# Performance work log

Hardware: AMD Instinct MI355X
Metric: run time of the kernel (lower is better)

## Reference

```python
import math
import jax, jax.numpy as jnp
import numpy as np

B, T, S = 4, 4096, 1024
HID, CTX, EMB, H = 1024, 768, 1024, 16
D = EMB // H  # head_dim = 64


def setup_inputs() -> dict:
    key = jax.random.key(0)
    ks = jax.random.split(key, 7)
    sc = lambda n: 1.0 / math.sqrt(n)
    return {
        "tokens": jax.random.normal(ks[0], (B, T, HID), jnp.float32),
        "context": jax.random.normal(ks[1], (B, S, CTX), jnp.float32),
        "Wq": jax.random.normal(ks[2], (HID, EMB), jnp.float32) * sc(HID),
        "Wk": jax.random.normal(ks[3], (CTX, EMB), jnp.float32) * sc(CTX),
        "Wv": jax.random.normal(ks[4], (CTX, EMB), jnp.float32) * sc(CTX),
        "Wo": jax.random.normal(ks[5], (EMB, HID), jnp.float32) * sc(EMB),
        "bo": jnp.zeros((HID,), jnp.float32),
    }


def reference(tokens, context, Wq, Wk, Wv, Wo, bo):
    # projections (bias-free, as in torch Linear(bias=False))
    Q = tokens @ Wq              # [B,T,EMB]
    K = context @ Wk             # [B,S,EMB]
    V = context @ Wv             # [B,S,EMB]
    # split heads: B T (H D) -> B H T D
    Q = Q.reshape(B, T, H, D).transpose(0, 2, 1, 3)
    K = K.reshape(B, S, H, D).transpose(0, 2, 1, 3)
    V = V.reshape(B, S, H, D).transpose(0, 2, 1, 3)
    scores = jnp.einsum('bhtd,bhsd->bhts', Q, K) / math.sqrt(D)
    attn = jax.nn.softmax(scores, axis=-1)
    ctx = jnp.einsum('bhts,bhsd->bhtd', attn, V)
    ctx = ctx.transpose(0, 2, 1, 3).reshape(B, T, EMB)
    return ctx @ Wo + bo
```

## Files before the change

kernel.cpp:

```cpp
#include <hip/hip_runtime.h>
#include <hip/hip_bf16.h>

#define B_ 4
#define T_ 4096
#define S_ 1024
#define HID_ 1024
#define CTX_ 768
#define EMB_ 1024
#define H_ 16
#define D_ 64

#define QSCALE 0.18033688011112042f

typedef __attribute__((ext_vector_type(8))) short short8;
typedef __attribute__((ext_vector_type(4))) float f32x4;
typedef __attribute__((ext_vector_type(4))) unsigned short us4;
typedef unsigned short ushort_t;

__device__ inline ushort_t f2b(float f) {
  union { float f; unsigned u; } x; x.f = f;
  return (ushort_t)((x.u + 0x7fffu + ((x.u >> 16) & 1u)) >> 16);
}
__device__ inline unsigned cvtpk2(float a, float b) {
  __hip_bfloat162 h = __float22bfloat162_rn(float2{a, b});
  union { __hip_bfloat162 h; unsigned u; } c; c.h = h; return c.u;
}
__device__ inline ushort_t f2b_fast(float f) {
  __hip_bfloat16 h = __float2bfloat16(f);
  union { __hip_bfloat16 h; ushort_t u; } c; c.h = h; return c.u;
}

using gu32p = const __attribute__((address_space(1))) unsigned int*;
using lu32p = __attribute__((address_space(3))) unsigned int*;
__device__ inline void gload16(const ushort_t* g, ushort_t* l) {
  __builtin_amdgcn_global_load_lds((gu32p)(const void*)g, (lu32p)(void*)l, 16, 0, 0);
}

__device__ inline void conv_body(const float* __restrict__ in, ushort_t* __restrict__ out,
                                 int blk, int tid) {
  const size_t i = ((size_t)blk * 256 + tid) * 8;
  const float4 a = *(const float4*)(in + i);
  const float4 b = *(const float4*)(in + i + 4);
  uint4 u;
  u.x = cvtpk2(a.x, a.y); u.y = cvtpk2(a.z, a.w);
  u.z = cvtpk2(b.x, b.y); u.w = cvtpk2(b.z, b.w);
  *(uint4*)(out + i) = u;
}

__device__ inline void convT_body(const float* __restrict__ W, ushort_t* __restrict__ Wt,
                                  int K, int tile, int tid, float (*Ls)[33]) {
  const int n0 = (tile & 31) * 32, k0 = (tile >> 5) * 32;
  const int r = tid >> 3, c4 = (tid & 7) * 4;
  const float4 v = *(const float4*)&W[(size_t)(k0 + r) * 1024 + n0 + c4];
  Ls[r][c4] = v.x; Ls[r][c4 + 1] = v.y; Ls[r][c4 + 2] = v.z; Ls[r][c4 + 3] = v.w;
  __syncthreads();
  us4 o;
  o.x = f2b_fast(Ls[c4][r]);     o.y = f2b_fast(Ls[c4 + 1][r]);
  o.z = f2b_fast(Ls[c4 + 2][r]); o.w = f2b_fast(Ls[c4 + 3][r]);
  *(us4*)&Wt[(size_t)(n0 + r) * K + k0 + c4] = o;
}

__global__ __launch_bounds__(256) void prepA(
    const float* __restrict__ context,
    const float* __restrict__ Wq, const float* __restrict__ Wk,
    const float* __restrict__ Wv, const float* __restrict__ Wo,
    ushort_t* __restrict__ CtxB, ushort_t* __restrict__ WqT,
    ushort_t* __restrict__ WkvT, ushort_t* __restrict__ WoT)
{
  __shared__ float Ls[32][33];
  const int tid = threadIdx.x;
  int blk = (int)blockIdx.x;
  if (blk < 1536) { conv_body(context, CtxB, blk, tid); return; }
  blk -= 1536;
  if (blk < 1024) { convT_body(Wq, WqT, 1024, blk, tid, Ls); return; }
  blk -= 1024;
  if (blk < 768)  { convT_body(Wk, WkvT, 768, blk, tid, Ls); return; }
  blk -= 768;
  if (blk < 768)  { convT_body(Wv, WkvT + (size_t)1024 * 768, 768, blk, tid, Ls); return; }
  blk -= 768;
  convT_body(Wo, WoT, 1024, blk, tid, Ls);
}

__global__ __launch_bounds__(512) void gemm256kv(
    const ushort_t* __restrict__ A, const ushort_t* __restrict__ Bt,
    ushort_t* __restrict__ Kb, ushort_t* __restrict__ Vtb)
{
  constexpr int Kd = CTX_, NT = CTX_ / 32;
  extern __shared__ ushort_t L[];
  const int tid = threadIdx.x;
  const int lane = tid & 63, wid = tid >> 6;
  const int lr = lane & 15, lg = lane >> 4;
  const int wm = wid >> 2, wn = wid & 3;

  const int lin = (int)blockIdx.x;
  const int swz = (lin & 7) * 32 + (lin >> 3);
  const int bm = swz >> 3, bn = swz & 7;

  const int sr = tid >> 2;
  const int csrc = (tid & 3) ^ ((sr >> 1) & 3);
  const ushort_t* gA = A + (size_t)(bm * 128 + sr) * Kd + csrc * 8;
  const ushort_t* gB = Bt + (size_t)(bn * 256 + sr) * Kd + csrc * 8;
  const size_t halfB = (size_t)128 * Kd;

  f32x4 acc[4][4] = {};

#define KVSTAGE(c, slot) do { const int k0_ = (c) << 5;            \
    ushort_t* s_ = L + (slot) * 12288;                             \
    gload16(gA + k0_, s_ + tid * 8);                               \
    gload16(gB + k0_, s_ + 4096 + tid * 8);                        \
    gload16(gB + k0_ + halfB, s_ + 8192 + tid * 8);                \
  } while (0)

  KVSTAGE(0, 0); KVSTAGE(1, 1);
  int cur = 0, sls = 2;
  for (int t = 0; t < NT; ++t) {
    if (t < NT - 1) asm volatile("s_waitcnt vmcnt(3)" ::: "memory");
    else            asm volatile("s_waitcnt vmcnt(0)" ::: "memory");
    __builtin_amdgcn_s_barrier();
    __builtin_amdgcn_sched_barrier(0);
    if (t + 2 < NT) KVSTAGE(t + 2, sls);
    const ushort_t* As_ = L + cur * 12288;
    const ushort_t* Bs_ = As_ + 4096;
    short8 af[4], bf[4];
#pragma unroll
    for (int m = 0; m < 4; ++m) {
      const int row = wm * 64 + m * 16 + lr;
      af[m] = *(const short8*)&As_[row * 32 + (lg ^ ((row >> 1) & 3)) * 8];
    }
#pragma unroll
    for (int n = 0; n < 4; ++n) {
      const int row = wn * 64 + n * 16 + lr;
      bf[n] = *(const short8*)&Bs_[row * 32 + (lg ^ ((row >> 1) & 3)) * 8];
    }
    __builtin_amdgcn_s_setprio(1);
#pragma unroll
    for (int m = 0; m < 4; ++m)
#pragma unroll
      for (int n = 0; n < 4; ++n)
        acc[m][n] = __builtin_amdgcn_mfma_f32_16x16x32_bf16(af[m], bf[n], acc[m][n], 0, 0, 0);
    __builtin_amdgcn_s_setprio(0);
    cur = (cur == 2) ? 0 : cur + 1;
    sls = (sls == 2) ? 0 : sls + 1;
  }
#undef KVSTAGE

  const int row0 = bm * 128 + wm * 64 + lg * 4;
  const int col0 = bn * 256 + wn * 64 + lr;

  if (col0 < 1024) {
#pragma unroll
    for (int m = 0; m < 4; ++m)
#pragma unroll
      for (int n = 0; n < 4; ++n) {
        const int col = col0 + n * 16;
#pragma unroll
        for (int i = 0; i < 4; ++i)
          Kb[(size_t)(row0 + m * 16 + i) * EMB_ + col] = f2b_fast(acc[m][n][i]);
      }
  } else {
#pragma unroll
    for (int m = 0; m < 4; ++m) {
      const int rbase = row0 + m * 16;
      const int bb = rbase >> 10;
      const int s0 = rbase & (S_ - 1);
#pragma unroll
      for (int n = 0; n < 4; ++n) {
        const int vc = col0 + n * 16 - 1024;
        const int hh = vc >> 6, dd = vc & 63;
        us4 o;
        o.x = f2b_fast(acc[m][n][0]); o.y = f2b_fast(acc[m][n][1]);
        o.z = f2b_fast(acc[m][n][2]); o.w = f2b_fast(acc[m][n][3]);
        *(us4*)&Vtb[(((size_t)bb * H_ + hh) * D_ + dd) * S_ + s0] = o;
      }
    }
  }
}

__global__ __launch_bounds__(512) void gemm256p(
    const ushort_t* __restrict__ A, const ushort_t* __restrict__ Bt,
    float* __restrict__ Cp, const float* __restrict__ bias,
    int M, int Kd, int N)
{
  extern __shared__ ushort_t L[];
  const int tid = threadIdx.x;
  const int lane = tid & 63, wid = tid >> 6;
  const int lr = lane & 15, lg = lane >> 4;
  const int wm = wid >> 2, wn = wid & 3;

  const int cpx = (int)gridDim.x >> 3;
  const int lin = (int)blockIdx.x;
  const int swz = (lin & 7) * cpx + (lin >> 3);
  const int nbn = N >> 8;
  const int bm = swz / nbn, bn = swz % nbn;

  const int sr = tid >> 2;
  const int csrc = (tid & 3) ^ ((sr >> 1) & 3);
  const ushort_t* gA = A + (size_t)(bm * 256 + sr) * Kd + csrc * 8;
  const ushort_t* gB = Bt + (size_t)(bn * 256 + sr) * Kd + csrc * 8;
  const size_t half = (size_t)128 * Kd;

  f32x4 acc[8][4] = {};
  const int NT = Kd >> 5;

#define STAGEQ(c, q) do {                                            \
    const int k0_ = (c) << 5;                                        \
    ushort_t* s_ = L + ((c) % 3) * 16384 + (q) * 4096 + tid * 8;     \
    if ((q) == 0)      gload16(gA + k0_, s_);                        \
    else if ((q) == 1) gload16(gA + k0_ + half, s_);                 \
    else if ((q) == 2) gload16(gB + k0_, s_);                        \
    else               gload16(gB + k0_ + half, s_);                 \
  } while (0)

#pragma unroll
  for (int q = 0; q < 4; ++q) STAGEQ(0, q);
#pragma unroll
  for (int q = 0; q < 4; ++q) STAGEQ(1, q);
  asm volatile("s_waitcnt vmcnt(4)" ::: "memory");
  __builtin_amdgcn_s_barrier();
  __builtin_amdgcn_sched_barrier(0);

  for (int t = 0; t < NT; ++t) {
    const ushort_t* As_ = L + (t % 3) * 16384;
    const ushort_t* Bs_ = As_ + 8192;
    const bool st = (t + 2 < NT);
    short8 bf[4];
#pragma unroll
    for (int q = 0; q < 4; ++q) {
      if (q == 0) {
#pragma unroll
        for (int n = 0; n < 4; ++n) {
          const int row = wn * 64 + n * 16 + lr;
          bf[n] = *(const short8*)&Bs_[row * 32 + (lg ^ ((row >> 1) & 3)) * 8];
        }
      }
      const int r0 = wm * 128 + (2 * q) * 16 + lr;
      const int r1 = r0 + 16;
      const short8 af0 = *(const short8*)&As_[r0 * 32 + (lg ^ ((r0 >> 1) & 3)) * 8];
      const short8 af1 = *(const short8*)&As_[r1 * 32 + (lg ^ ((r1 >> 1) & 3)) * 8];
      if (st) STAGEQ(t + 2, q);
      __builtin_amdgcn_s_barrier();
      asm volatile("s_waitcnt lgkmcnt(0)" ::: "memory");
      __builtin_amdgcn_sched_barrier(0);
      __builtin_amdgcn_s_setprio(1);
#pragma unroll
      for (int n = 0; n < 4; ++n)
        acc[2 * q][n] = __builtin_amdgcn_mfma_f32_16x16x32_bf16(af0, bf[n], acc[2 * q][n], 0, 0, 0);
#pragma unroll
      for (int n = 0; n < 4; ++n)
        acc[2 * q + 1][n] = __builtin_amdgcn_mfma_f32_16x16x32_bf16(af1, bf[n], acc[2 * q + 1][n], 0, 0, 0);
      __builtin_amdgcn_s_setprio(0);
      if (q == 3 && t < NT - 1) {
        if (st) asm volatile("s_waitcnt vmcnt(4)" ::: "memory");
        else    asm volatile("s_waitcnt vmcnt(0)" ::: "memory");
      }
      __builtin_amdgcn_s_barrier();
      __builtin_amdgcn_sched_barrier(0);
    }
  }
#undef STAGEQ

  const int row0 = bm * 256 + wm * 128 + lg * 4;
  const int col0 = bn * 256 + wn * 64 + lr;
#pragma unroll
  for (int n = 0; n < 4; ++n) {
    const int col = col0 + n * 16;
    const float bv = bias[col];
#pragma unroll
    for (int m = 0; m < 8; ++m)
#pragma unroll
      for (int i = 0; i < 4; ++i)
        Cp[(size_t)(row0 + m * 16 + i) * N + col] = acc[m][n][i] + bv;
  }
}

__global__ __launch_bounds__(512) void gemm256f(
    const float* __restrict__ Af, const ushort_t* __restrict__ Bt,
    ushort_t* __restrict__ Cp, int M, int N)
{
  constexpr int Kd = 1024, NT = 32;
  extern __shared__ ushort_t L[];
  const int tid = threadIdx.x;
  const int lane = tid & 63, wid = tid >> 6;
  const int lr = lane & 15, lg = lane >> 4;
  const int wm = wid >> 2, wn = wid & 3;

  const int cpx = (int)gridDim.x >> 3;
  const int lin = (int)blockIdx.x;
  const int swz = (lin & 7) * cpx + (lin >> 3);
  const int nbn = N >> 8;
  const int bm = swz / nbn, bn = swz % nbn;

  const int sr = tid >> 2;
  const int csrc = (tid & 3) ^ ((sr >> 1) & 3);
  const float* gA = Af + (size_t)(bm * 256 + sr) * Kd + csrc * 8;
  const ushort_t* gB = Bt + (size_t)(bn * 256 + sr) * Kd + csrc * 8;
  const size_t half = (size_t)128 * Kd;
  ushort_t* const dA = L + tid * 8;
  ushort_t* const dB = L + 8192 + tid * 8;

  f32x4 acc[8][4] = {};
  float4 ra0[4], ra1[4];

#define ALOADF(c, RS) do { const int k0_ = (c) << 5;      \
    RS[0] = *(const float4*)(gA + k0_);                   \
    RS[1] = *(const float4*)(gA + k0_ + 4);               \
    RS[2] = *(const float4*)(gA + k0_ + half);            \
    RS[3] = *(const float4*)(gA + k0_ + half + 4);        \
  } while (0)

#define AWRITE(c, RS) do { const int slot_ = ((c) & 3) * 16384;  \
    uint4 u0, u1;                                                \
    u0.x = cvtpk2(RS[0].x, RS[0].y); u0.y = cvtpk2(RS[0].z, RS[0].w); \
    u0.z = cvtpk2(RS[1].x, RS[1].y); u0.w = cvtpk2(RS[1].z, RS[1].w); \
    u1.x = cvtpk2(RS[2].x, RS[2].y); u1.y = cvtpk2(RS[2].z, RS[2].w); \
    u1.z = cvtpk2(RS[3].x, RS[3].y); u1.w = cvtpk2(RS[3].z, RS[3].w); \
    *(uint4*)(dA + slot_) = u0;                                  \
    *(uint4*)(dA + slot_ + 4096) = u1;                           \
  } while (0)

#define BSTAGE(c) do { const int slot_ = ((c) & 3) * 16384; const int k0_ = (c) << 5; \
    gload16(gB + k0_, dB + slot_);                      \
    gload16(gB + k0_ + half, dB + slot_ + 4096);        \
  } while (0)

#define COMPUTE(c) do {                                                  \
    const ushort_t* As_ = L + ((c) & 3) * 16384;                         \
    const ushort_t* Bs_ = As_ + 8192;                                    \
    short8 af[8], bf[4];                                                 \
    _Pragma("unroll")                                                    \
    for (int m = 0; m < 8; ++m) {                                        \
      const int row = wm * 128 + m * 16 + lr;                            \
      af[m] = *(const short8*)&As_[row * 32 + (lg ^ ((row >> 1) & 3)) * 8]; \
    }                                                                    \
    _Pragma("unroll")                                                    \
    for (int n = 0; n < 4; ++n) {                                        \
      const int row = wn * 64 + n * 16 + lr;                             \
      bf[n] = *(const short8*)&Bs_[row * 32 + (lg ^ ((row >> 1) & 3)) * 8]; \
    }                                                                    \
    __builtin_amdgcn_s_setprio(1);                                       \
    _Pragma("unroll")                                                    \
    for (int m = 0; m < 8; ++m)                                          \
      _Pragma("unroll")                                                  \
      for (int n = 0; n < 4; ++n)                                        \
        acc[m][n] = __builtin_amdgcn_mfma_f32_16x16x32_bf16(af[m], bf[n], acc[m][n], 0, 0, 0); \
    __builtin_amdgcn_s_setprio(0);                                       \
  } while (0)

#define ENDBAR do {                                        \
    asm volatile("s_waitcnt lgkmcnt(0)" ::: "memory");     \
    __builtin_amdgcn_s_barrier();                          \
    __builtin_amdgcn_sched_barrier(0);                     \
  } while (0)

  {
    float4 p0[4], p1[4], p2[4];
    ALOADF(0, p0); ALOADF(1, p1); ALOADF(2, p2);
    AWRITE(0, p0); AWRITE(1, p1); AWRITE(2, p2);
    BSTAGE(0); BSTAGE(1); BSTAGE(2);
    ALOADF(3, ra1);
    asm volatile("s_waitcnt vmcnt(4)" ::: "memory");
    ENDBAR;
  }

  for (int t = 0; t < NT; t += 2) {
    if (t + 3 < NT) { AWRITE(t + 3, ra1); BSTAGE(t + 3); }
    if (t + 4 < NT) ALOADF(t + 4, ra0);
    COMPUTE(t);
    ENDBAR;
    if (t + 4 < NT) { AWRITE(t + 4, ra0); BSTAGE(t + 4); }
    if (t + 5 < NT) ALOADF(t + 5, ra1);
    COMPUTE(t + 1);
    ENDBAR;
  }
#undef ALOADF
#undef AWRITE
#undef BSTAGE
#undef COMPUTE
#undef ENDBAR

  const int row0 = bm * 256 + wm * 128 + lg * 4;
  const int col0 = bn * 256 + wn * 64 + lr;
#pragma unroll
  for (int m = 0; m < 8; ++m)
#pragma unroll
    for (int n = 0; n < 4; ++n) {
      const int col = col0 + n * 16;
#pragma unroll
      for (int i = 0; i < 4; ++i)
        Cp[(size_t)(row0 + m * 16 + i) * N + col] = f2b(acc[m][n][i] * QSCALE);
    }
}

__global__ __launch_bounds__(512) void attn_v8(
    const ushort_t* __restrict__ Q, const ushort_t* __restrict__ K,
    const ushort_t* __restrict__ Vt, ushort_t* __restrict__ C)
{
  extern __shared__ ushort_t SM[];
  const int tid = threadIdx.x;
  const int lane = tid & 63, w = tid >> 6;
  const int lr = lane & 15, lg = lane >> 4;

  const int bid = (int)blockIdx.x;
  const int g = (bid & 7) | (((bid >> 3) >> 4) << 3);
  const int tb = (bid >> 3) & 15;
  const int h = g & 15, b = g >> 4;
  const int t0 = tb * 256;

  short8 qf[2][2];
#pragma unroll
  for (int qs = 0; qs < 2; ++qs) {
    const size_t qrow = (size_t)b * T_ + t0 + w * 32 + qs * 16 + lr;
    const ushort_t* qp = Q + qrow * EMB_ + h * 64;
    qf[qs][0] = *(const short8*)(qp + lg * 8);
    qf[qs][1] = *(const short8*)(qp + 32 + lg * 8);
  }

  short8 ones;
#pragma unroll
  for (int j = 0; j < 8; ++j) ones[j] = (short)0x3F80;

  f32x4 o[2][4] = {};
  f32x4 lacc[2] = {};

  const int srow = tid >> 3, schunk = tid & 7;
  const int sswz = schunk ^ (srow & 7);
  const ushort_t* kg = K + ((size_t)b * S_ + srow) * EMB_ + h * 64 + sswz * 8;
  const ushort_t* vg = Vt + (((size_t)b * H_ + h) * D_ + srow) * S_ + sswz * 8;
  ushort_t* Psw = SM + 24576 + w * 1152;

  gload16(kg, SM + tid * 8);
  gload16(vg, SM + 12288 + tid * 8);
  gload16(kg + (size_t)64 * EMB_, SM + 4096 + tid * 8);
  gload16(vg + 64, SM + 12288 + 4096 + tid * 8);

  int cur = 0, sls = 2;
  for (int st = 0; st < 16; ++st) {
    if (st < 15) asm volatile("s_waitcnt vmcnt(2)" ::: "memory");
    else         asm volatile("s_waitcnt vmcnt(0)" ::: "memory");
    __builtin_amdgcn_s_barrier();
    __builtin_amdgcn_sched_barrier(0);
    if (st + 2 < 16) {
      gload16(kg + (size_t)(st + 2) * 64 * EMB_, SM + sls * 4096 + tid * 8);
      gload16(vg + (st + 2) * 64, SM + 12288 + sls * 4096 + tid * 8);
    }
    const ushort_t* Ksb = SM + cur * 4096;
    const ushort_t* Vsb = SM + 12288 + cur * 4096;

    f32x4 sacc[2][4] = {};
    __builtin_amdgcn_s_setprio(1);
#pragma unroll
    for (int c = 0; c < 4; ++c) {
      const int krow = c * 16 + lr;
      const int sw = krow & 7;
      const short8 ka0 = *(const short8*)&Ksb[krow * 64 + ((lg ^ sw) * 8)];
      const short8 ka1 = *(const short8*)&Ksb[krow * 64 + (((4 + lg) ^ sw) * 8)];
#pragma unroll
      for (int qs = 0; qs < 2; ++qs) {
        sacc[qs][c] = __builtin_amdgcn_mfma_f32_16x16x32_bf16(ka0, qf[qs][0], sacc[qs][c], 0, 0, 0);
        sacc[qs][c] = __builtin_amdgcn_mfma_f32_16x16x32_bf16(ka1, qf[qs][1], sacc[qs][c], 0, 0, 0);
      }
    }
    __builtin_amdgcn_s_setprio(0);

    short8 pa[2][2];
#pragma unroll
    for (int qs = 0; qs < 2; ++qs) {
#pragma unroll
      for (int c = 0; c < 4; ++c) {
        uint2 pk;
        pk.x = cvtpk2(exp2f(sacc[qs][c][0]), exp2f(sacc[qs][c][1]));
        pk.y = cvtpk2(exp2f(sacc[qs][c][2]), exp2f(sacc[qs][c][3]));
        *(uint2*)&Psw[lr * 72 + c * 16 + lg * 4] = pk;
      }
      pa[qs][0] = *(const short8*)&Psw[lr * 72 + lg * 8];
      pa[qs][1] = *(const short8*)&Psw[lr * 72 + 32 + lg * 8];
    }

    __builtin_amdgcn_s_setprio(1);
#pragma unroll
    for (int sh = 0; sh < 2; ++sh) {
#pragma unroll
      for (int dc = 0; dc < 4; ++dc) {
        const int vrow = dc * 16 + lr;
        const int vsw = vrow & 7;
        const short8 vb = *(const short8*)&Vsb[vrow * 64 + (((sh * 4 + lg) ^ vsw) * 8)];
        o[0][dc] = __builtin_amdgcn_mfma_f32_16x16x32_bf16(pa[0][sh], vb, o[0][dc], 0, 0, 0);
        o[1][dc] = __builtin_amdgcn_mfma_f32_16x16x32_bf16(pa[1][sh], vb, o[1][dc], 0, 0, 0);
      }
      lacc[0] = __builtin_amdgcn_mfma_f32_16x16x32_bf16(pa[0][sh], ones, lacc[0], 0, 0, 0);
      lacc[1] = __builtin_amdgcn_mfma_f32_16x16x32_bf16(pa[1][sh], ones, lacc[1], 0, 0, 0);
    }
    __builtin_amdgcn_s_setprio(0);

    cur = (cur == 2) ? 0 : cur + 1;
    sls = (sls == 2) ? 0 : sls + 1;
  }

#pragma unroll
  for (int qs = 0; qs < 2; ++qs) {
#pragma unroll
    for (int i = 0; i < 4; ++i) {
      const float li = 1.0f / lacc[qs][i];
      const size_t trow = (size_t)b * T_ + t0 + w * 32 + qs * 16 + lg * 4 + i;
#pragma unroll
      for (int dc = 0; dc < 4; ++dc)
        C[trow * EMB_ + h * 64 + dc * 16 + lr] = f2b_fast(o[qs][dc][i] * li);
    }
  }
}

extern "C" void kernel_launch(void* const* d_in, const int* in_sizes, int n_in,
                              void* d_out, int out_size, void* d_ws, size_t ws_size,
                              hipStream_t stream) {
  const float* tokens  = (const float*)d_in[0];
  const float* context = (const float*)d_in[1];
  const float* Wq = (const float*)d_in[2];
  const float* Wk = (const float*)d_in[3];
  const float* Wv = (const float*)d_in[4];
  const float* Wo = (const float*)d_in[5];
  const float* bo = (const float*)d_in[6];
  float* out = (float*)d_out;

  ushort_t* Qb  = (ushort_t*)d_out;
  ushort_t* Kb   = (ushort_t*)d_ws;
  ushort_t* Vtb  = Kb + (size_t)B_ * S_ * EMB_;
  ushort_t* Cb   = Vtb + (size_t)B_ * S_ * EMB_;
  ushort_t* WqT  = Cb + (size_t)B_ * T_ * EMB_;
  ushort_t* WkvT = WqT + (size_t)EMB_ * HID_;
  ushort_t* WoT  = WkvT + (size_t)EMB_ * 2 * CTX_;

  prepA<<<5120, 256, 0, stream>>>(context, Wq, Wk, Wv, Wo, Cb, WqT, WkvT, WoT);
  gemm256f<<<dim3((B_ * T_ / 256) * (EMB_ / 256)), 512, 131072, stream>>>(
      tokens, WqT, Qb, B_ * T_, EMB_);
  gemm256kv<<<dim3(256), 512, 73728, stream>>>(Cb, WkvT, Kb, Vtb);
  attn_v8<<<dim3((T_ / 256) * H_ * B_), 512, 67584, stream>>>(Qb, Kb, Vtb, Cb);
  gemm256p<<<dim3((B_ * T_ / 256) * (HID_ / 256)), 512, 98304, stream>>>(
      Cb, WoT, out, bo, B_ * T_, EMB_, HID_);
}
```

Measured before the change: 224.9 us.

## Fuse Q and KV projections into one launch, converting context to bf16 in-kernel

Drops the separate fp32→bf16 conversion of the context tensor from the prep kernel. The KV projection now loads fp32 context through registers, converts it, and writes it to LDS, like the Q projection already does. The Q and KV GEMMs become device functions dispatched by interleaved block index in one proj2 kernel with 512 blocks, which removes a launch and lets the smaller KV GEMM fill the idle CUs. The Q pipeline tail is restructured to drain the last two tiles after a full vmcnt wait. In exchange, every block now reserves the larger Q shared-memory footprint.

```diff
diff --git a/kernel.cpp b/kernel.cpp
--- a/kernel.cpp
+++ b/kernel.cpp
@@ -34,17 +34,6 @@
 using lu32p = __attribute__((address_space(3))) unsigned int*;
 __device__ inline void gload16(const ushort_t* g, ushort_t* l) {
   __builtin_amdgcn_global_load_lds((gu32p)(const void*)g, (lu32p)(void*)l, 16, 0, 0);
-}
-
-__device__ inline void conv_body(const float* __restrict__ in, ushort_t* __restrict__ out,
-                                 int blk, int tid) {
-  const size_t i = ((size_t)blk * 256 + tid) * 8;
-  const float4 a = *(const float4*)(in + i);
-  const float4 b = *(const float4*)(in + i + 4);
-  uint4 u;
-  u.x = cvtpk2(a.x, a.y); u.y = cvtpk2(a.z, a.w);
-  u.z = cvtpk2(b.x, b.y); u.w = cvtpk2(b.z, b.w);
-  *(uint4*)(out + i) = u;
 }
 
 __device__ inline void convT_body(const float* __restrict__ W, ushort_t* __restrict__ Wt,
@@ -61,17 +50,14 @@
 }
 
 __global__ __launch_bounds__(256) void prepA(
-    const float* __restrict__ context,
     const float* __restrict__ Wq, const float* __restrict__ Wk,
     const float* __restrict__ Wv, const float* __restrict__ Wo,
-    ushort_t* __restrict__ CtxB, ushort_t* __restrict__ WqT,
-    ushort_t* __restrict__ WkvT, ushort_t* __restrict__ WoT)
+    ushort_t* __restrict__ WqT, ushort_t* __restrict__ WkvT,
+    ushort_t* __restrict__ WoT)
 {
   __shared__ float Ls[32][33];
   const int tid = threadIdx.x;
   int blk = (int)blockIdx.x;
-  if (blk < 1536) { conv_body(context, CtxB, blk, tid); return; }
-  blk -= 1536;
   if (blk < 1024) { convT_body(Wq, WqT, 1024, blk, tid, Ls); return; }
   blk -= 1024;
   if (blk < 768)  { convT_body(Wk, WkvT, 768, blk, tid, Ls); return; }
@@ -81,214 +67,19 @@
   convT_body(Wo, WoT, 1024, blk, tid, Ls);
 }
 
-__global__ __launch_bounds__(512) void gemm256kv(
-    const ushort_t* __restrict__ A, const ushort_t* __restrict__ Bt,
-    ushort_t* __restrict__ Kb, ushort_t* __restrict__ Vtb)
+
+__device__ __forceinline__ void q_body(
+    int lin, int tid, ushort_t* L,
+    const float* __restrict__ Af, const ushort_t* __restrict__ Bt,
+    ushort_t* __restrict__ Cp)
 {
-  constexpr int Kd = CTX_, NT = CTX_ / 32;
-  extern __shared__ ushort_t L[];
-  const int tid = threadIdx.x;
+  constexpr int Kd = 1024, NT = 32, N = EMB_;
   const int lane = tid & 63, wid = tid >> 6;
   const int lr = lane & 15, lg = lane >> 4;
   const int wm = wid >> 2, wn = wid & 3;
 
-  const int lin = (int)blockIdx.x;
   const int swz = (lin & 7) * 32 + (lin >> 3);
-  const int bm = swz >> 3, bn = swz & 7;
-
-  const int sr = tid >> 2;
-  const int csrc = (tid & 3) ^ ((sr >> 1) & 3);
-  const ushort_t* gA = A + (size_t)(bm * 128 + sr) * Kd + csrc * 8;
-  const ushort_t* gB = Bt + (size_t)(bn * 256 + sr) * Kd + csrc * 8;
-  const size_t halfB = (size_t)128 * Kd;
-
-  f32x4 acc[4][4] = {};
-
-#define KVSTAGE(c, slot) do { const int k0_ = (c) << 5;            \
-    ushort_t* s_ = L + (slot) * 12288;                             \
-    gload16(gA + k0_, s_ + tid * 8);                               \
-    gload16(gB + k0_, s_ + 4096 + tid * 8);                        \
-    gload16(gB + k0_ + halfB, s_ + 8192 + tid * 8);                \
-  } while (0)
-
-  KVSTAGE(0, 0); KVSTAGE(1, 1);
-  int cur = 0, sls = 2;
-  for (int t = 0; t < NT; ++t) {
-    if (t < NT - 1) asm volatile("s_waitcnt vmcnt(3)" ::: "memory");
-    else            asm volatile("s_waitcnt vmcnt(0)" ::: "memory");
-    __builtin_amdgcn_s_barrier();
-    __builtin_amdgcn_sched_barrier(0);
-    if (t + 2 < NT) KVSTAGE(t + 2, sls);
-    const ushort_t* As_ = L + cur * 12288;
-    const ushort_t* Bs_ = As_ + 4096;
-    short8 af[4], bf[4];
-#pragma unroll
-    for (int m = 0; m < 4; ++m) {
-      const int row = wm * 64 + m * 16 + lr;
-      af[m] = *(const short8*)&As_[row * 32 + (lg ^ ((row >> 1) & 3)) * 8];
-    }
-#pragma unroll
-    for (int n = 0; n < 4; ++n) {
-      const int row = wn * 64 + n * 16 + lr;
-      bf[n] = *(const short8*)&Bs_[row * 32 + (lg ^ ((row >> 1) & 3)) * 8];
-    }
-    __builtin_amdgcn_s_setprio(1);
-#pragma unroll
-    for (int m = 0; m < 4; ++m)
-#pragma unroll
-      for (int n = 0; n < 4; ++n)
-        acc[m][n] = __builtin_amdgcn_mfma_f32_16x16x32_bf16(af[m], bf[n], acc[m][n], 0, 0, 0);
-    __builtin_amdgcn_s_setprio(0);
-    cur = (cur == 2) ? 0 : cur + 1;
-    sls = (sls == 2) ? 0 : sls + 1;
-  }
-#undef KVSTAGE
-
-  const int row0 = bm * 128 + wm * 64 + lg * 4;
-  const int col0 = bn * 256 + wn * 64 + lr;
-
-  if (col0 < 1024) {
-#pragma unroll
-    for (int m = 0; m < 4; ++m)
-#pragma unroll
-      for (int n = 0; n < 4; ++n) {
-        const int col = col0 + n * 16;
-#pragma unroll
-        for (int i = 0; i < 4; ++i)
-          Kb[(size_t)(row0 + m * 16 + i) * EMB_ + col] = f2b_fast(acc[m][n][i]);
-      }
-  } else {
-#pragma unroll
-    for (int m = 0; m < 4; ++m) {
-      const int rbase = row0 + m * 16;
-      const int bb = rbase >> 10;
-      const int s0 = rbase & (S_ - 1);
-#pragma unroll
-      for (int n = 0; n < 4; ++n) {
-        const int vc = col0 + n * 16 - 1024;
-        const int hh = vc >> 6, dd = vc & 63;
-        us4 o;
-        o.x = f2b_fast(acc[m][n][0]); o.y = f2b_fast(acc[m][n][1]);
-        o.z = f2b_fast(acc[m][n][2]); o.w = f2b_fast(acc[m][n][3]);
-        *(us4*)&Vtb[(((size_t)bb * H_ + hh) * D_ + dd) * S_ + s0] = o;
-      }
-    }
-  }
-}
-
-__global__ __launch_bounds__(512) void gemm256p(
-    const ushort_t* __restrict__ A, const ushort_t* __restrict__ Bt,
-    float* __restrict__ Cp, const float* __restrict__ bias,
-    int M, int Kd, int N)
-{
-  extern __shared__ ushort_t L[];
-  const int tid = threadIdx.x;
-  const int lane = tid & 63, wid = tid >> 6;
-  const int lr = lane & 15, lg = lane >> 4;
-  const int wm = wid >> 2, wn = wid & 3;
-
-  const int cpx = (int)gridDim.x >> 3;
-  const int lin = (int)blockIdx.x;
-  const int swz = (lin & 7) * cpx + (lin >> 3);
-  const int nbn = N >> 8;
-  const int bm = swz / nbn, bn = swz % nbn;
-
-  const int sr = tid >> 2;
-  const int csrc = (tid & 3) ^ ((sr >> 1) & 3);
-  const ushort_t* gA = A + (size_t)(bm * 256 + sr) * Kd + csrc * 8;
-  const ushort_t* gB = Bt + (size_t)(bn * 256 + sr) * Kd + csrc * 8;
-  const size_t half = (size_t)128 * Kd;
-
-  f32x4 acc[8][4] = {};
-  const int NT = Kd >> 5;
-
-#define STAGEQ(c, q) do {                                            \
-    const int k0_ = (c) << 5;                                        \
-    ushort_t* s_ = L + ((c) % 3) * 16384 + (q) * 4096 + tid * 8;     \
-    if ((q) == 0)      gload16(gA + k0_, s_);                        \
-    else if ((q) == 1) gload16(gA + k0_ + half, s_);                 \
-    else if ((q) == 2) gload16(gB + k0_, s_);                        \
-    else               gload16(gB + k0_ + half, s_);                 \
-  } while (0)
-
-#pragma unroll
-  for (int q = 0; q < 4; ++q) STAGEQ(0, q);
-#pragma unroll
-  for (int q = 0; q < 4; ++q) STAGEQ(1, q);
-  asm volatile("s_waitcnt vmcnt(4)" ::: "memory");
-  __builtin_amdgcn_s_barrier();
-  __builtin_amdgcn_sched_barrier(0);
-
-  for (int t = 0; t < NT; ++t) {
-    const ushort_t* As_ = L + (t % 3) * 16384;
-    const ushort_t* Bs_ = As_ + 8192;
-    const bool st = (t + 2 < NT);
-    short8 bf[4];
-#pragma unroll
-    for (int q = 0; q < 4; ++q) {
-      if (q == 0) {
-#pragma unroll
-        for (int n = 0; n < 4; ++n) {
-          const int row = wn * 64 + n * 16 + lr;
-          bf[n] = *(const short8*)&Bs_[row * 32 + (lg ^ ((row >> 1) & 3)) * 8];
-        }
-      }
-      const int r0 = wm * 128 + (2 * q) * 16 + lr;
-      const int r1 = r0 + 16;
-      const short8 af0 = *(const short8*)&As_[r0 * 32 + (lg ^ ((r0 >> 1) & 3)) * 8];
-      const short8 af1 = *(const short8*)&As_[r1 * 32 + (lg ^ ((r1 >> 1) & 3)) * 8];
-      if (st) STAGEQ(t + 2, q);
-      __builtin_amdgcn_s_barrier();
-      asm volatile("s_waitcnt lgkmcnt(0)" ::: "memory");
-      __builtin_amdgcn_sched_barrier(0);
-      __builtin_amdgcn_s_setprio(1);
-#pragma unroll
-      for (int n = 0; n < 4; ++n)
-        acc[2 * q][n] = __builtin_amdgcn_mfma_f32_16x16x32_bf16(af0, bf[n], acc[2 * q][n], 0, 0, 0);
-#pragma unroll
-      for (int n = 0; n < 4; ++n)
-        acc[2 * q + 1][n] = __builtin_amdgcn_mfma_f32_16x16x32_bf16(af1, bf[n], acc[2 * q + 1][n], 0, 0, 0);
-      __builtin_amdgcn_s_setprio(0);
-      if (q == 3 && t < NT - 1) {
-        if (st) asm volatile("s_waitcnt vmcnt(4)" ::: "memory");
-        else    asm volatile("s_waitcnt vmcnt(0)" ::: "memory");
-      }
-      __builtin_amdgcn_s_barrier();
-      __builtin_amdgcn_sched_barrier(0);
-    }
-  }
-#undef STAGEQ
-
-  const int row0 = bm * 256 + wm * 128 + lg * 4;
-  const int col0 = bn * 256 + wn * 64 + lr;
-#pragma unroll
-  for (int n = 0; n < 4; ++n) {
-    const int col = col0 + n * 16;
-    const float bv = bias[col];
-#pragma unroll
-    for (int m = 0; m < 8; ++m)
-#pragma unroll
-      for (int i = 0; i < 4; ++i)
-        Cp[(size_t)(row0 + m * 16 + i) * N + col] = acc[m][n][i] + bv;
-  }
-}
-
-__global__ __launch_bounds__(512) void gemm256f(
-    const float* __restrict__ Af, const ushort_t* __restrict__ Bt,
-    ushort_t* __restrict__ Cp, int M, int N)
-{
-  constexpr int Kd = 1024, NT = 32;
-  extern __shared__ ushort_t L[];
-  const int tid = threadIdx.x;
-  const int lane = tid & 63, wid = tid >> 6;
-  const int lr = lane & 15, lg = lane >> 4;
-  const int wm = wid >> 2, wn = wid & 3;
-
-  const int cpx = (int)gridDim.x >> 3;
-  const int lin = (int)blockIdx.x;
-  const int swz = (lin & 7) * cpx + (lin >> 3);
-  const int nbn = N >> 8;
-  const int bm = swz / nbn, bn = swz % nbn;
+  const int bm = swz >> 2, bn = swz & 3;
 
   const int sr = tid >> 2;
   const int csrc = (tid & 3) ^ ((sr >> 1) & 3);
@@ -362,7 +153,7 @@
     ENDBAR;
   }
 
-  for (int t = 0; t < NT; t += 2) {
+  for (int t = 0; t < NT - 2; t += 2) {
     if (t + 3 < NT) { AWRITE(t + 3, ra1); BSTAGE(t + 3); }
     if (t + 4 < NT) ALOADF(t + 4, ra0);
     COMPUTE(t);
@@ -372,6 +163,11 @@
     COMPUTE(t + 1);
     ENDBAR;
   }
+  asm volatile("s_waitcnt vmcnt(0)" ::: "memory");
+  __builtin_amdgcn_s_barrier();
+  __builtin_amdgcn_sched_barrier(0);
+  COMPUTE(NT - 2);
+  COMPUTE(NT - 1);
 #undef ALOADF
 #undef AWRITE
 #undef BSTAGE
@@ -389,6 +185,246 @@
       for (int i = 0; i < 4; ++i)
         Cp[(size_t)(row0 + m * 16 + i) * N + col] = f2b(acc[m][n][i] * QSCALE);
     }
+}
+
+__device__ __forceinline__ void kv_body(
+    int lin, int tid, ushort_t* L,
+    const float* __restrict__ Ctx, const ushort_t* __restrict__ Bt,
+    ushort_t* __restrict__ Kb, ushort_t* __restrict__ Vtb)
+{
+  constexpr int Kd = CTX_, NT = CTX_ / 32;
+  const int lane = tid & 63, wid = tid >> 6;
+  const int lr = lane & 15, lg = lane >> 4;
+  const int wm = wid >> 2, wn = wid & 3;
+
+  const int swz = (lin & 7) * 32 + (lin >> 3);
+  const int bm = swz >> 3, bn = swz & 7;
+
+  const int sr = tid >> 2;
+  const int csrc = (tid & 3) ^ ((sr >> 1) & 3);
+  const float* gA = Ctx + (size_t)(bm * 128 + sr) * Kd + csrc * 8;
+  const ushort_t* gB = Bt + (size_t)(bn * 256 + sr) * Kd + csrc * 8;
+  const size_t halfB = (size_t)128 * Kd;
+
+  f32x4 acc[4][4] = {};
+  float4 ra0[2], ra1[2];
+
+#define ALOADF2(c, RS) do { const int k0_ = (c) << 5;     \
+    RS[0] = *(const float4*)(gA + k0_);                   \
+    RS[1] = *(const float4*)(gA + k0_ + 4);               \
+  } while (0)
+
+#define AWRITE2(c, RS) do { const int slot_ = ((c) % 3) * 12288;  \
+    uint4 u0;                                                     \
+    u0.x = cvtpk2(RS[0].x, RS[0].y); u0.y = cvtpk2(RS[0].z, RS[0].w); \
+    u0.z = cvtpk2(RS[1].x, RS[1].y); u0.w = cvtpk2(RS[1].z, RS[1].w); \
+    *(uint4*)(L + slot_ + tid * 8) = u0;                          \
+  } while (0)
+
+#define BSTAGE2(c) do { const int slot_ = ((c) % 3) * 12288; const int k0_ = (c) << 5; \
+    gload16(gB + k0_, L + slot_ + 4096 + tid * 8);              \
+    gload16(gB + k0_ + halfB, L + slot_ + 8192 + tid * 8);      \
+  } while (0)
+
+#define COMPUTEKV(c) do {                                                \
+    const ushort_t* As_ = L + ((c) % 3) * 12288;                         \
+    const ushort_t* Bs_ = As_ + 4096;                                    \
+    short8 af[4], bf[4];                                                 \
+    _Pragma("unroll")                                                    \
+    for (int m = 0; m < 4; ++m) {                                        \
+      const int row = wm * 64 + m * 16 + lr;                             \
+      af[m] = *(const short8*)&As_[row * 32 + (lg ^ ((row >> 1) & 3)) * 8]; \
+    }                                                                    \
+    _Pragma("unroll")                                                    \
+    for (int n = 0; n < 4; ++n) {                                        \
+      const int row = wn * 64 + n * 16 + lr;                             \
+      bf[n] = *(const short8*)&Bs_[row * 32 + (lg ^ ((row >> 1) & 3)) * 8]; \
+    }                                                                    \
+    __builtin_amdgcn_s_setprio(1);                                       \
+    _Pragma("unroll")                                                    \
+    for (int m = 0; m < 4; ++m)                                          \
+      _Pragma("unroll")                                                  \
+      for (int n = 0; n < 4; ++n)                                        \
+        acc[m][n] = __builtin_amdgcn_mfma_f32_16x16x32_bf16(af[m], bf[n], acc[m][n], 0, 0, 0); \
+    __builtin_amdgcn_s_setprio(0);                                       \
+  } while (0)
+
+#define ENDBAR2 do {                                       \
+    asm volatile("s_waitcnt lgkmcnt(0)" ::: "memory");     \
+    __builtin_amdgcn_s_barrier();                          \
+    __builtin_amdgcn_sched_barrier(0);                     \
+  } while (0)
+
+  {
+    float4 p0[2], p1[2];
+    ALOADF2(0, p0); ALOADF2(1, p1);
+    AWRITE2(0, p0); AWRITE2(1, p1);
+    BSTAGE2(0); BSTAGE2(1);
+    ALOADF2(2, ra0);
+    asm volatile("s_waitcnt vmcnt(2)" ::: "memory");
+    ENDBAR2;
+  }
+
+  for (int t = 0; t < NT - 2; t += 2) {
+    AWRITE2(t + 2, ra0); BSTAGE2(t + 2);
+    if (t + 3 < NT) ALOADF2(t + 3, ra1);
+    COMPUTEKV(t);
+    ENDBAR2;
+    AWRITE2(t + 3, ra1); BSTAGE2(t + 3);
+    if (t + 4 < NT) ALOADF2(t + 4, ra0);
+    COMPUTEKV(t + 1);
+    ENDBAR2;
+  }
+  asm volatile("s_waitcnt vmcnt(0)" ::: "memory");
+  __builtin_amdgcn_s_barrier();
+  __builtin_amdgcn_sched_barrier(0);
+  COMPUTEKV(NT - 2);
+  COMPUTEKV(NT - 1);
+#undef ALOADF2
+#undef AWRITE2
+#undef BSTAGE2
+#undef COMPUTEKV
+#undef ENDBAR2
+
+  const int row0 = bm * 128 + wm * 64 + lg * 4;
+  const int col0 = bn * 256 + wn * 64 + lr;
+
+  if (col0 < 1024) {
+#pragma unroll
+    for (int m = 0; m < 4; ++m)
+#pragma unroll
+      for (int n = 0; n < 4; ++n) {
+        const int col = col0 + n * 16;
+#pragma unroll
+        for (int i = 0; i < 4; ++i)
+          Kb[(size_t)(row0 + m * 16 + i) * EMB_ + col] = f2b_fast(acc[m][n][i]);
+      }
+  } else {
+#pragma unroll
+    for (int m = 0; m < 4; ++m) {
+      const int rbase = row0 + m * 16;
+      const int bb = rbase >> 10;
+      const int s0 = rbase & (S_ - 1);
+#pragma unroll
+      for (int n = 0; n < 4; ++n) {
+        const int vc = col0 + n * 16 - 1024;
+        const int hh = vc >> 6, dd = vc & 63;
+        us4 o;
+        o.x = f2b_fast(acc[m][n][0]); o.y = f2b_fast(acc[m][n][1]);
+        o.z = f2b_fast(acc[m][n][2]); o.w = f2b_fast(acc[m][n][3]);
+        *(us4*)&Vtb[(((size_t)bb * H_ + hh) * D_ + dd) * S_ + s0] = o;
+      }
+    }
+  }
+}
+
+__global__ __launch_bounds__(512) void proj2(
+    const float* __restrict__ tokens, const float* __restrict__ ctx,
+    const ushort_t* __restrict__ WqT, const ushort_t* __restrict__ WkvT,
+    ushort_t* __restrict__ Qb, ushort_t* __restrict__ Kb,
+    ushort_t* __restrict__ Vtb)
+{
+  extern __shared__ ushort_t L[];
+  const int blk = (int)blockIdx.x;
+  if (blk & 1) kv_body(blk >> 1, threadIdx.x, L, ctx, WkvT, Kb, Vtb);
+  else         q_body(blk >> 1, threadIdx.x, L, tokens, WqT, Qb);
+}
+
+__global__ __launch_bounds__(512) void gemm256p(
+    const ushort_t* __restrict__ A, const ushort_t* __restrict__ Bt,
+    float* __restrict__ Cp, const float* __restrict__ bias,
+    int M, int Kd, int N)
+{
+  extern __shared__ ushort_t L[];
+  const int tid = threadIdx.x;
+  const int lane = tid & 63, wid = tid >> 6;
+  const int lr = lane & 15, lg = lane >> 4;
+  const int wm = wid >> 2, wn = wid & 3;
+
+  const int cpx = (int)gridDim.x >> 3;
+  const int lin = (int)blockIdx.x;
+  const int swz = (lin & 7) * cpx + (lin >> 3);
+  const int nbn = N >> 8;
+  const int bm = swz / nbn, bn = swz % nbn;
+
+  const int sr = tid >> 2;
+  const int csrc = (tid & 3) ^ ((sr >> 1) & 3);
+  const ushort_t* gA = A + (size_t)(bm * 256 + sr) * Kd + csrc * 8;
+  const ushort_t* gB = Bt + (size_t)(bn * 256 + sr) * Kd + csrc * 8;
+  const size_t half = (size_t)128 * Kd;
+
+  f32x4 acc[8][4] = {};
+  const int NT = Kd >> 5;
+
+#define STAGEQ(c, q) do {                                            \
+    const int k0_ = (c) << 5;                                        \
+    ushort_t* s_ = L + ((c) % 3) * 16384 + (q) * 4096 + tid * 8;     \
+    if ((q) == 0)      gload16(gA + k0_, s_);                        \
+    else if ((q) == 1) gload16(gA + k0_ + half, s_);                 \
+    else if ((q) == 2) gload16(gB + k0_, s_);                        \
+    else               gload16(gB + k0_ + half, s_);                 \
+  } while (0)
+
+#pragma unroll
+  for (int q = 0; q < 4; ++q) STAGEQ(0, q);
+#pragma unroll
+  for (int q = 0; q < 4; ++q) STAGEQ(1, q);
+  asm volatile("s_waitcnt vmcnt(4)" ::: "memory");
+  __builtin_amdgcn_s_barrier();
+  __builtin_amdgcn_sched_barrier(0);
+
+  for (int t = 0; t < NT; ++t) {
+    const ushort_t* As_ = L + (t % 3) * 16384;
+    const ushort_t* Bs_ = As_ + 8192;
+    const bool st = (t + 2 < NT);
+    short8 bf[4];
+#pragma unroll
+    for (int q = 0; q < 4; ++q) {
+      if (q == 0) {
+#pragma unroll
+        for (int n = 0; n < 4; ++n) {
+          const int row = wn * 64 + n * 16 + lr;
+          bf[n] = *(const short8*)&Bs_[row * 32 + (lg ^ ((row >> 1) & 3)) * 8];
+        }
+      }
+      const int r0 = wm * 128 + (2 * q) * 16 + lr;
+      const int r1 = r0 + 16;
+      const short8 af0 = *(const short8*)&As_[r0 * 32 + (lg ^ ((r0 >> 1) & 3)) * 8];
+      const short8 af1 = *(const short8*)&As_[r1 * 32 + (lg ^ ((r1 >> 1) & 3)) * 8];
+      if (st) STAGEQ(t + 2, q);
+      __builtin_amdgcn_s_barrier();
+      asm volatile("s_waitcnt lgkmcnt(0)" ::: "memory");
+      __builtin_amdgcn_sched_barrier(0);
+      __builtin_amdgcn_s_setprio(1);
+#pragma unroll
+      for (int n = 0; n < 4; ++n)
+        acc[2 * q][n] = __builtin_amdgcn_mfma_f32_16x16x32_bf16(af0, bf[n], acc[2 * q][n], 0, 0, 0);
+#pragma unroll
+      for (int n = 0; n < 4; ++n)
+        acc[2 * q + 1][n] = __builtin_amdgcn_mfma_f32_16x16x32_bf16(af1, bf[n], acc[2 * q + 1][n], 0, 0, 0);
+      __builtin_amdgcn_s_setprio(0);
+      if (q == 3 && t < NT - 1) {
+        if (st) asm volatile("s_waitcnt vmcnt(4)" ::: "memory");
+        else    asm volatile("s_waitcnt vmcnt(0)" ::: "memory");
+      }
+      __builtin_amdgcn_s_barrier();
+      __builtin_amdgcn_sched_barrier(0);
+    }
+  }
+#undef STAGEQ
+
+  const int row0 = bm * 256 + wm * 128 + lg * 4;
+  const int col0 = bn * 256 + wn * 64 + lr;
+#pragma unroll
+  for (int n = 0; n < 4; ++n) {
+    const int col = col0 + n * 16;
+    const float bv = bias[col];
+#pragma unroll
+    for (int m = 0; m < 8; ++m)
+#pragma unroll
+      for (int i = 0; i < 4; ++i)
+        Cp[(size_t)(row0 + m * 16 + i) * N + col] = acc[m][n][i] + bv;
+  }
 }
 
 __global__ __launch_bounds__(512) void attn_v8(
@@ -529,10 +565,8 @@
   ushort_t* WkvT = WqT + (size_t)EMB_ * HID_;
   ushort_t* WoT  = WkvT + (size_t)EMB_ * 2 * CTX_;
 
-  prepA<<<5120, 256, 0, stream>>>(context, Wq, Wk, Wv, Wo, Cb, WqT, WkvT, WoT);
-  gemm256f<<<dim3((B_ * T_ / 256) * (EMB_ / 256)), 512, 131072, stream>>>(
-      tokens, WqT, Qb, B_ * T_, EMB_);
-  gemm256kv<<<dim3(256), 512, 73728, stream>>>(Cb, WkvT, Kb, Vtb);
+  prepA<<<3584, 256, 0, stream>>>(Wq, Wk, Wv, Wo, WqT, WkvT, WoT);
+  proj2<<<512, 512, 131072, stream>>>(tokens, context, WqT, WkvT, Qb, Kb, Vtb);
   attn_v8<<<dim3((T_ / 256) * H_ * B_), 512, 67584, stream>>>(Qb, Kb, Vtb, Cb);
   gemm256p<<<dim3((B_ * T_ / 256) * (HID_ / 256)), 512, 98304, stream>>>(
       Cb, WoT, out, bo, B_ * T_, EMB_, HID_);
```

After: 241.1 us. +7.2%, slower.
